# Kernel optimization log

Measured on AMD Instinct MI355X. Metric: run time of the kernel, lower is better.

## Reference

```python
import jax, jax.numpy as jnp
import numpy as np
from jax import lax

EPS = 1e-8

def _conv(x, w, b):
    # x: [B,Cin,H,W], w: [Cout,Cin,kh,kw] (torch OIHW layout), SAME padding, stride 1
    y = lax.conv_general_dilated(x, w, (1, 1), 'SAME',
                                 dimension_numbers=('NCHW', 'OIHW', 'NCHW'))
    return y + b[None, :, None, None]

def setup_inputs() -> dict:
    key = jax.random.key(0)
    ks = jax.random.split(key, 16)
    B, S, H, A, NZ, NO = 256, 4, 32, 5, 150, 17
    d = {
        'map_in': jax.random.uniform(ks[0], (B, 2, H, H), jnp.float32),
        'b0': jax.random.uniform(ks[1], (B, H, H), jnp.float32),
        'act_in': jax.random.randint(ks[2], (B, S), 0, A),
        'obs_in': jax.random.uniform(ks[3], (B, S, 4), jnp.float32),
        'is_start': 1,
        'step_size': S,
        'VI_k': 64,
        # parameters, initialized per the torch init scheme
        'Tb_w': 1.0 / 9.0 + jax.random.normal(ks[4], (A, 1, 3, 3)) / 90.0,
        'Tb_b': jnp.zeros((A,)),
        'Tv_w': 1.0 / 9.0 + jax.random.normal(ks[5], (A, 1, 3, 3)) / 90.0,
        'Tv_b': jnp.zeros((A,)),
        'Z1_w': jax.random.normal(ks[6], (NZ, 1, 3, 3)) / 3.0,
        'Z1_b': jnp.zeros((NZ,)),
        'Z2_w': jax.random.normal(ks[7], (NO, NZ, 1, 1)) / np.sqrt(NZ),
        'Z2_b': jnp.zeros((NO,)),
        'O1_w': jax.random.normal(ks[8], (NO, 4)) * 0.25,
        'O1_b': jnp.zeros((NO,)),
        'O3_w': jax.random.normal(ks[9], (NO, NO)) / NO,
        'O3_b': jnp.zeros((NO,)),
        'R1_w': jax.random.normal(ks[10], (NZ, 2, 3, 3)) / np.sqrt(18.0),
        'R1_b': jnp.zeros((NZ,)),
        'R2_w': jax.random.normal(ks[11], (A, NZ, 1, 1)) / np.sqrt(NZ),
        'R2_b': jnp.zeros((A,)),
        'FL_w': jax.random.normal(ks[12], (A, A)) * 0.25,
        'FL_b': jnp.zeros((A,)),
    }
    return d

def reference(map_in, b0, act_in, obs_in, is_start, step_size, VI_k,
              Tb_w, Tb_b, Tv_w, Tv_b, Z1_w, Z1_b, Z2_w, Z2_b,
              O1_w, O1_b, O3_w, O3_b, R1_w, R1_b, R2_w, R2_b, FL_w, FL_b):
    B, _, H, W = map_in.shape
    A = Tb_w.shape[0]

    # ---- VI: value iteration conv+add+max loop ----
    R = _conv(jax.nn.relu(_conv(map_in, R1_w, R1_b)), R2_w, R2_b)  # [B,A,H,W]
    v0 = jnp.zeros((B, 1, H, W), map_in.dtype)
    Q0 = jnp.zeros_like(R)

    def vi_step(carry, _):
        v, _Q = carry
        Q = _conv(v, Tv_w, Tv_b) + R
        v = jnp.max(Q, axis=1, keepdims=True)
        return (v, Q), None

    (_, Q), _ = lax.scan(vi_step, (v0, Q0), None, length=VI_k)
    Q = jnp.transpose(Q, (0, 2, 3, 1))  # [B,H,W,A]

    # ---- observation model Z ----
    Z = jax.nn.sigmoid(_conv(_conv(map_in[:, :1], Z1_w, Z1_b), Z2_w, Z2_b))
    Z = jnp.transpose(Z, (0, 2, 3, 1))  # [B,H,W,17]
    Z = Z / (jnp.sum(Z, axis=3, keepdims=True) + EPS)

    # ---- recurrent Bayes filter + policy ----
    b = b0 if is_start else b0  # is_start resets belief to b0 (always true here)
    outs = []
    for t in range(step_size):  # small fixed recurrence length
        o = obs_in[:, t]  # [B,4]
        w = jax.nn.softmax(jnp.tanh(o @ O1_w.T + O1_b) @ O3_w.T + O3_b, axis=1)  # [B,17]
        Z_O = jnp.einsum('bhwo,bo->bhw', Z, w)
        bp = jnp.transpose(_conv(b[:, None], Tb_w, Tb_b), (0, 2, 3, 1))  # [B,H,W,A]
        a1h = jax.nn.one_hot(act_in[:, t], A, dtype=bp.dtype)
        b_pa = jnp.einsum('bhwa,ba->bhw', bp, a1h)
        b_next = b_pa * Z_O
        b = b_next / (jnp.sum(b_next, axis=(1, 2), keepdims=True) + EPS)
        Qb = jnp.einsum('bhwa,bhw->ba', Q, b)
        outs.append(Qb @ FL_w.T + FL_b)
    outputs = jnp.concatenate(outs, axis=0)  # [step_size*B, A]
    return outputs, b
```

## Files before the change

kernel.cpp:

```cpp
#include <hip/hip_runtime.h>

#define EPSV 1e-8f
#define PW   34
#define NPIX 1024
#define NA   5
#define NOUT 17
#define NZC  150
#define MAXS 8

__global__ __launch_bounds__(1024, 4) void vin_fused(
    const float* __restrict__ map_in, const float* __restrict__ b0,
    const int*   __restrict__ act_in, const float* __restrict__ obs_in,
    const int*   __restrict__ step_p, const int*   __restrict__ vik_p,
    const float* __restrict__ Tb_w,  const float* __restrict__ Tb_b,
    const float* __restrict__ Tv_w,  const float* __restrict__ Tv_b,
    const float* __restrict__ Z1_w,  const float* __restrict__ Z1_b,
    const float* __restrict__ Z2_w,  const float* __restrict__ Z2_b,
    const float* __restrict__ O1_w,  const float* __restrict__ O1_b,
    const float* __restrict__ O3_w,  const float* __restrict__ O3_b,
    const float* __restrict__ R1_w,  const float* __restrict__ R1_b,
    const float* __restrict__ R2_w,  const float* __restrict__ R2_b,
    const float* __restrict__ FL_w,  const float* __restrict__ FL_b,
    float* __restrict__ out, int B)
{
    __shared__ float map0[PW*PW], map1[PW*PW], v_lds[PW*PW], b_lds[PW*PW];
    __shared__ float zc_w[NOUT*9], zc_b[NOUT];
    __shared__ float h_all[MAXS][NOUT], u_all[MAXS][NOUT], w_all[MAXS][NOUT];
    __shared__ float zo_lds[MAXS * NPIX];
    __shared__ float partials[16][6], sums[6];

    const int tid  = threadIdx.x;
    const int blk  = blockIdx.x;
    const int y    = tid >> 5, x = tid & 31;
    const int pidx = (y + 1) * PW + (x + 1);
    const int lane = tid & 63, wvid = tid >> 6;

    const int S = step_p[0];
    const int K = vik_p[0];

    for (int i = tid; i < PW*PW; i += NPIX) {
        map0[i] = 0.f; map1[i] = 0.f; v_lds[i] = 0.f; b_lds[i] = 0.f;
    }
    __syncthreads();
    map0[pidx]  = map_in[blk*2*NPIX + tid];
    map1[pidx]  = map_in[blk*2*NPIX + NPIX + tid];
    b_lds[pidx] = b0[blk*NPIX + tid];

    if (tid < NOUT*9) {
        const int o = tid / 9, k = tid % 9;
        float s = 0.f;
        for (int c = 0; c < NZC; ++c) s += Z2_w[o*NZC + c] * Z1_w[c*9 + k];
        zc_w[tid] = s;
    } else if (tid < NOUT*9 + NOUT) {
        const int o = tid - NOUT*9;
        float s = Z2_b[o];
        for (int c = 0; c < NZC; ++c) s += Z2_w[o*NZC + c] * Z1_b[c];
        zc_b[o] = s;
    }

    const int mt = tid - 256;
    const int mT = mt / NOUT, mO = mt % NOUT;
    if (mt >= 0 && mt < S*NOUT) {
        const float* ob = obs_in + (blk*S + mT)*4;
        float hh = O1_b[mO];
        #pragma unroll
        for (int k = 0; k < 4; ++k) hh += ob[k] * O1_w[mO*4 + k];
        h_all[mT][mO] = tanhf(hh);
    }
    __syncthreads();
    if (mt >= 0 && mt < S*NOUT) {
        float u = O3_b[mO];
        #pragma unroll
        for (int j = 0; j < NOUT; ++j) u += h_all[mT][j] * O3_w[mO*NOUT + j];
        u_all[mT][mO] = u;
    }
    __syncthreads();
    if (mt >= 0 && mt < S*NOUT) {
        float mx = u_all[mT][0];
        #pragma unroll
        for (int j = 1; j < NOUT; ++j) mx = fmaxf(mx, u_all[mT][j]);
        float sm = 0.f;
        #pragma unroll
        for (int j = 0; j < NOUT; ++j) sm += expf(u_all[mT][j] - mx);
        w_all[mT][mO] = expf(u_all[mT][mO] - mx) / sm;
    }
    __syncthreads();

    float m0[9], m1[9];
    #pragma unroll
    for (int k = 0; k < 9; ++k) {
        const int off = (y + k/3)*PW + x + (k%3);
        m0[k] = map0[off]; m1[k] = map1[off];
    }

    float r[NA];
    #pragma unroll
    for (int a = 0; a < NA; ++a) r[a] = R2_b[a];
    for (int c = 0; c < NZC; ++c) {
        float s = R1_b[c];
        const float* w1 = R1_w + c*18;
        #pragma unroll
        for (int k = 0; k < 9; ++k) s += m0[k] * w1[k];
        #pragma unroll
        for (int k = 0; k < 9; ++k) s += m1[k] * w1[9 + k];
        s = fmaxf(s, 0.f);
        #pragma unroll
        for (int a = 0; a < NA; ++a) r[a] += R2_w[a*NZC + c] * s;
    }

    {
        float z[NOUT];
        float zs = 0.f;
        #pragma unroll
        for (int o = 0; o < NOUT; ++o) {
            float s = zc_b[o];
            #pragma unroll
            for (int k = 0; k < 9; ++k) s += m0[k] * zc_w[o*9 + k];
            const float zz = 1.f / (1.f + expf(-s));
            z[o] = zz; zs += zz;
        }
        const float zn = 1.f / (zs + EPSV);
        for (int t = 0; t < S; ++t) {
            float zo = 0.f;
            #pragma unroll
            for (int o = 0; o < NOUT; ++o) zo += z[o] * w_all[t][o];
            zo_lds[t*NPIX + tid] = zo * zn;
        }
    }

    float q[NA];
    #pragma unroll
    for (int a = 0; a < NA; ++a) q[a] = 0.f;
    for (int it = 0; it < K; ++it) {
        float n[9];
        #pragma unroll
        for (int k = 0; k < 9; ++k) n[k] = v_lds[(y + k/3)*PW + x + (k%3)];
        float vmax = -3.4e38f;
        #pragma unroll
        for (int a = 0; a < NA; ++a) {
            float s = Tv_b[a] + r[a];
            #pragma unroll
            for (int k = 0; k < 9; ++k) s += n[k] * Tv_w[a*9 + k];
            q[a] = s;
            vmax = fmaxf(vmax, s);
        }
        __syncthreads();
        v_lds[pidx] = vmax;
        __syncthreads();
    }

    for (int t = 0; t < S; ++t) {
        const int a_t = act_in[blk*S + t];
        float bp = Tb_b[a_t];
        #pragma unroll
        for (int k = 0; k < 9; ++k)
            bp += b_lds[(y + k/3)*PW + x + (k%3)] * Tb_w[a_t*9 + k];

        const float bn = bp * zo_lds[t*NPIX + tid];

        float v6[6];
        v6[5] = bn;
        #pragma unroll
        for (int a = 0; a < NA; ++a) v6[a] = q[a] * bn;
        #pragma unroll
        for (int k = 0; k < 6; ++k) {
            float vv = v6[k];
            for (int off = 32; off > 0; off >>= 1) vv += __shfl_down(vv, off);
            v6[k] = vv;
        }
        if (lane == 0) {
            #pragma unroll
            for (int k = 0; k < 6; ++k) partials[wvid][k] = v6[k];
        }
        __syncthreads();
        if (tid < 6) {
            float s = 0.f;
            for (int w2 = 0; w2 < 16; ++w2) s += partials[w2][tid];
            sums[tid] = s;
        }
        __syncthreads();

        const float inv = 1.f / (sums[5] + EPSV);
        if (tid < NA) {
            float oj = FL_b[tid];
            #pragma unroll
            for (int a = 0; a < NA; ++a) oj += (sums[a] * inv) * FL_w[tid*NA + a];
            out[(t*B + blk)*NA + tid] = oj;
        }
        b_lds[pidx] = bn * inv;
        __syncthreads();
    }

    out[S*B*NA + blk*NPIX + tid] = b_lds[pidx];
}

extern "C" void kernel_launch(void* const* d_in, const int* in_sizes, int n_in,
                              void* d_out, int out_size, void* d_ws, size_t ws_size,
                              hipStream_t stream)
{
    const float* map_in = (const float*)d_in[0];
    const float* b0     = (const float*)d_in[1];
    const int*   act_in = (const int*)  d_in[2];
    const float* obs_in = (const float*)d_in[3];
    const int*   step_p = (const int*)  d_in[5];
    const int*   vik_p  = (const int*)  d_in[6];
    const float* Tb_w = (const float*)d_in[7];
    const float* Tb_b = (const float*)d_in[8];
    const float* Tv_w = (const float*)d_in[9];
    const float* Tv_b = (const float*)d_in[10];
    const float* Z1_w = (const float*)d_in[11];
    const float* Z1_b = (const float*)d_in[12];
    const float* Z2_w = (const float*)d_in[13];
    const float* Z2_b = (const float*)d_in[14];
    const float* O1_w = (const float*)d_in[15];
    const float* O1_b = (const float*)d_in[16];
    const float* O3_w = (const float*)d_in[17];
    const float* O3_b = (const float*)d_in[18];
    const float* R1_w = (const float*)d_in[19];
    const float* R1_b = (const float*)d_in[20];
    const float* R2_w = (const float*)d_in[21];
    const float* R2_b = (const float*)d_in[22];
    const float* FL_w = (const float*)d_in[23];
    const float* FL_b = (const float*)d_in[24];

    const int B = in_sizes[1] / NPIX;

    hipLaunchKernelGGL(vin_fused, dim3(B), dim3(1024), 0, stream,
        map_in, b0, act_in, obs_in, step_p, vik_p,
        Tb_w, Tb_b, Tv_w, Tv_b, Z1_w, Z1_b, Z2_w, Z2_b,
        O1_w, O1_b, O3_w, O3_b, R1_w, R1_b, R2_w, R2_b,
        FL_w, FL_b, (float*)d_out, B);
}
```

Baseline: 187.9 us.

## Compute two vertically adjacent pixels per thread with double-buffered value map

Halves the block to 512 threads, with each thread computing two vertically stacked pixels. Overlapping stencil loads are shared between the two outputs, and each thread's own center values stay in registers. The value-iteration loop now ping-pongs between two LDS buffers, which cuts it to one barrier per iteration instead of two. Register pressure goes up, and there are fewer threads per block to hide latency.

```diff
diff --git a/kernel.cpp b/kernel.cpp
--- a/kernel.cpp
+++ b/kernel.cpp
@@ -8,7 +8,7 @@
 #define NZC  150
 #define MAXS 8
 
-__global__ __launch_bounds__(1024, 4) void vin_fused(
+__global__ __launch_bounds__(512, 2) void vin_fused(
     const float* __restrict__ map_in, const float* __restrict__ b0,
     const int*   __restrict__ act_in, const float* __restrict__ obs_in,
     const int*   __restrict__ step_p, const int*   __restrict__ vik_p,
@@ -23,28 +23,38 @@
     const float* __restrict__ FL_w,  const float* __restrict__ FL_b,
     float* __restrict__ out, int B)
 {
-    __shared__ float map0[PW*PW], map1[PW*PW], v_lds[PW*PW], b_lds[PW*PW];
+    __shared__ float map0[PW*PW], map1[PW*PW];
+    __shared__ float v_a[PW*PW], v_b[PW*PW], b_lds[PW*PW];
     __shared__ float zc_w[NOUT*9], zc_b[NOUT];
     __shared__ float h_all[MAXS][NOUT], u_all[MAXS][NOUT], w_all[MAXS][NOUT];
     __shared__ float zo_lds[MAXS * NPIX];
-    __shared__ float partials[16][6], sums[6];
+    __shared__ float partials[8][6], sums[6];
 
     const int tid  = threadIdx.x;
     const int blk  = blockIdx.x;
-    const int y    = tid >> 5, x = tid & 31;
-    const int pidx = (y + 1) * PW + (x + 1);
+    const int x    = tid & 31;
+    const int yr   = tid >> 5;
+    const int y0   = yr * 2;
+    const int p0   = y0*32 + x, p1 = p0 + 32;
+    const int bi   = y0*PW + x;
+    const int ci0  = bi + PW + 1;
+    const int ci1  = bi + 2*PW + 1;
     const int lane = tid & 63, wvid = tid >> 6;
 
     const int S = step_p[0];
     const int K = vik_p[0];
 
-    for (int i = tid; i < PW*PW; i += NPIX) {
-        map0[i] = 0.f; map1[i] = 0.f; v_lds[i] = 0.f; b_lds[i] = 0.f;
+    for (int i = tid; i < PW*PW; i += 512) {
+        map0[i] = 0.f; map1[i] = 0.f; v_a[i] = 0.f; v_b[i] = 0.f; b_lds[i] = 0.f;
     }
     __syncthreads();
-    map0[pidx]  = map_in[blk*2*NPIX + tid];
-    map1[pidx]  = map_in[blk*2*NPIX + NPIX + tid];
-    b_lds[pidx] = b0[blk*NPIX + tid];
+    map0[ci0] = map_in[blk*2*NPIX + p0];
+    map0[ci1] = map_in[blk*2*NPIX + p1];
+    map1[ci0] = map_in[blk*2*NPIX + NPIX + p0];
+    map1[ci1] = map_in[blk*2*NPIX + NPIX + p1];
+    float bc0 = b0[blk*NPIX + p0];
+    float bc1 = b0[blk*NPIX + p1];
+    b_lds[ci0] = bc0; b_lds[ci1] = bc1;
 
     if (tid < NOUT*9) {
         const int o = tid / 9, k = tid % 9;
@@ -86,31 +96,36 @@
     }
     __syncthreads();
 
-    float m0[9], m1[9];
+    float m0[12], m1[12];
     #pragma unroll
-    for (int k = 0; k < 9; ++k) {
-        const int off = (y + k/3)*PW + x + (k%3);
-        m0[k] = map0[off]; m1[k] = map1[off];
-    }
-
-    float r[NA];
+    for (int kr = 0; kr < 4; ++kr)
+        #pragma unroll
+        for (int kc = 0; kc < 3; ++kc) {
+            const int off = bi + kr*PW + kc;
+            m0[kr*3+kc] = map0[off]; m1[kr*3+kc] = map1[off];
+        }
+
+    float r0a[NA], r1a[NA];
     #pragma unroll
-    for (int a = 0; a < NA; ++a) r[a] = R2_b[a];
+    for (int a = 0; a < NA; ++a) { r0a[a] = R2_b[a]; r1a[a] = R2_b[a]; }
     for (int c = 0; c < NZC; ++c) {
-        float s = R1_b[c];
         const float* w1 = R1_w + c*18;
-        #pragma unroll
-        for (int k = 0; k < 9; ++k) s += m0[k] * w1[k];
-        #pragma unroll
-        for (int k = 0; k < 9; ++k) s += m1[k] * w1[9 + k];
-        s = fmaxf(s, 0.f);
-        #pragma unroll
-        for (int a = 0; a < NA; ++a) r[a] += R2_w[a*NZC + c] * s;
+        float s0 = R1_b[c], s1 = R1_b[c];
+        #pragma unroll
+        for (int k = 0; k < 9; ++k) { s0 += m0[k]   * w1[k];   s1 += m0[3+k] * w1[k]; }
+        #pragma unroll
+        for (int k = 0; k < 9; ++k) { s0 += m1[k]   * w1[9+k]; s1 += m1[3+k] * w1[9+k]; }
+        s0 = fmaxf(s0, 0.f); s1 = fmaxf(s1, 0.f);
+        #pragma unroll
+        for (int a = 0; a < NA; ++a) {
+            r0a[a] += R2_w[a*NZC + c] * s0;
+            r1a[a] += R2_w[a*NZC + c] * s1;
+        }
     }
 
     {
-        float z[NOUT];
-        float zs = 0.f;
+        float z[NOUT]; float zs;
+        zs = 0.f;
         #pragma unroll
         for (int o = 0; o < NOUT; ++o) {
             float s = zc_b[o];
@@ -119,49 +134,101 @@
             const float zz = 1.f / (1.f + expf(-s));
             z[o] = zz; zs += zz;
         }
-        const float zn = 1.f / (zs + EPSV);
-        for (int t = 0; t < S; ++t) {
-            float zo = 0.f;
+        {
+            const float zn = 1.f / (zs + EPSV);
+            for (int t = 0; t < S; ++t) {
+                float zo = 0.f;
+                #pragma unroll
+                for (int o = 0; o < NOUT; ++o) zo += z[o] * w_all[t][o];
+                zo_lds[t*NPIX + p0] = zo * zn;
+            }
+        }
+        zs = 0.f;
+        #pragma unroll
+        for (int o = 0; o < NOUT; ++o) {
+            float s = zc_b[o];
             #pragma unroll
-            for (int o = 0; o < NOUT; ++o) zo += z[o] * w_all[t][o];
-            zo_lds[t*NPIX + tid] = zo * zn;
-        }
-    }
-
-    float q[NA];
+            for (int k = 0; k < 9; ++k) s += m0[3+k] * zc_w[o*9 + k];
+            const float zz = 1.f / (1.f + expf(-s));
+            z[o] = zz; zs += zz;
+        }
+        {
+            const float zn = 1.f / (zs + EPSV);
+            for (int t = 0; t < S; ++t) {
+                float zo = 0.f;
+                #pragma unroll
+                for (int o = 0; o < NOUT; ++o) zo += z[o] * w_all[t][o];
+                zo_lds[t*NPIX + p1] = zo * zn;
+            }
+        }
+    }
+
+    float q0[NA], q1[NA];
     #pragma unroll
-    for (int a = 0; a < NA; ++a) q[a] = 0.f;
-    for (int it = 0; it < K; ++it) {
-        float n[9];
-        #pragma unroll
-        for (int k = 0; k < 9; ++k) n[k] = v_lds[(y + k/3)*PW + x + (k%3)];
-        float vmax = -3.4e38f;
-        #pragma unroll
-        for (int a = 0; a < NA; ++a) {
-            float s = Tv_b[a] + r[a];
-            #pragma unroll
-            for (int k = 0; k < 9; ++k) s += n[k] * Tv_w[a*9 + k];
-            q[a] = s;
-            vmax = fmaxf(vmax, s);
-        }
-        __syncthreads();
-        v_lds[pidx] = vmax;
-        __syncthreads();
-    }
+    for (int a = 0; a < NA; ++a) {
+        q0[a] = 0.f; q1[a] = 0.f;
+        r0a[a] += Tv_b[a]; r1a[a] += Tv_b[a];
+    }
+    float vc0 = 0.f, vc1 = 0.f;
+
+#define VISTEP(SRC, DST)                                                        \
+    {                                                                           \
+        const float A0 = SRC[bi],        A1 = SRC[bi+1],        A2 = SRC[bi+2]; \
+        const float B0 = SRC[bi+PW],     B2 = SRC[bi+PW+2];                     \
+        const float C0 = SRC[bi+2*PW],   C2 = SRC[bi+2*PW+2];                   \
+        const float D0 = SRC[bi+3*PW],   D1 = SRC[bi+3*PW+1],   D2 = SRC[bi+3*PW+2]; \
+        float vm0 = -3.4e38f, vm1 = -3.4e38f;                                   \
+        _Pragma("unroll")                                                       \
+        for (int a = 0; a < NA; ++a) {                                          \
+            const float* w = Tv_w + a*9;                                        \
+            float s0 = r0a[a];                                                  \
+            s0 += A0*w[0]; s0 += A1*w[1]; s0 += A2*w[2];                        \
+            s0 += B0*w[3]; s0 += vc0*w[4]; s0 += B2*w[5];                       \
+            s0 += C0*w[6]; s0 += vc1*w[7]; s0 += C2*w[8];                       \
+            float s1 = r1a[a];                                                  \
+            s1 += B0*w[0]; s1 += vc0*w[1]; s1 += B2*w[2];                       \
+            s1 += C0*w[3]; s1 += vc1*w[4]; s1 += C2*w[5];                       \
+            s1 += D0*w[6]; s1 += D1*w[7]; s1 += D2*w[8];                        \
+            q0[a] = s0; q1[a] = s1;                                             \
+            vm0 = fmaxf(vm0, s0); vm1 = fmaxf(vm1, s1);                         \
+        }                                                                       \
+        vc0 = vm0; vc1 = vm1;                                                   \
+        DST[ci0] = vm0; DST[ci1] = vm1;                                         \
+        __syncthreads();                                                        \
+    }
+
+    {
+        int it = 0;
+        for (; it + 1 < K; it += 2) { VISTEP(v_a, v_b); VISTEP(v_b, v_a); }
+        if (it < K) { VISTEP(v_a, v_b); }
+    }
+#undef VISTEP
 
     for (int t = 0; t < S; ++t) {
         const int a_t = act_in[blk*S + t];
-        float bp = Tb_b[a_t];
-        #pragma unroll
-        for (int k = 0; k < 9; ++k)
-            bp += b_lds[(y + k/3)*PW + x + (k%3)] * Tb_w[a_t*9 + k];
-
-        const float bn = bp * zo_lds[t*NPIX + tid];
+        const float* tw = Tb_w + a_t*9;
+        const float tb = Tb_b[a_t];
+        float bp0 = tb, bp1 = tb;
+        {
+            const float A0 = b_lds[bi],      A1 = b_lds[bi+1],      A2 = b_lds[bi+2];
+            const float B0 = b_lds[bi+PW],   B2 = b_lds[bi+PW+2];
+            const float C0 = b_lds[bi+2*PW], C2 = b_lds[bi+2*PW+2];
+            const float D0 = b_lds[bi+3*PW], D1 = b_lds[bi+3*PW+1], D2 = b_lds[bi+3*PW+2];
+            bp0 += A0*tw[0]; bp0 += A1*tw[1]; bp0 += A2*tw[2];
+            bp0 += B0*tw[3]; bp0 += bc0*tw[4]; bp0 += B2*tw[5];
+            bp0 += C0*tw[6]; bp0 += bc1*tw[7]; bp0 += C2*tw[8];
+            bp1 += B0*tw[0]; bp1 += bc0*tw[1]; bp1 += B2*tw[2];
+            bp1 += C0*tw[3]; bp1 += bc1*tw[4]; bp1 += C2*tw[5];
+            bp1 += D0*tw[6]; bp1 += D1*tw[7]; bp1 += D2*tw[8];
+        }
+
+        const float bn0 = bp0 * zo_lds[t*NPIX + p0];
+        const float bn1 = bp1 * zo_lds[t*NPIX + p1];
 
         float v6[6];
-        v6[5] = bn;
-        #pragma unroll
-        for (int a = 0; a < NA; ++a) v6[a] = q[a] * bn;
+        v6[5] = bn0 + bn1;
+        #pragma unroll
+        for (int a = 0; a < NA; ++a) v6[a] = q0[a]*bn0 + q1[a]*bn1;
         #pragma unroll
         for (int k = 0; k < 6; ++k) {
             float vv = v6[k];
@@ -175,7 +242,7 @@
         __syncthreads();
         if (tid < 6) {
             float s = 0.f;
-            for (int w2 = 0; w2 < 16; ++w2) s += partials[w2][tid];
+            for (int w2 = 0; w2 < 8; ++w2) s += partials[w2][tid];
             sums[tid] = s;
         }
         __syncthreads();
@@ -187,11 +254,13 @@
             for (int a = 0; a < NA; ++a) oj += (sums[a] * inv) * FL_w[tid*NA + a];
             out[(t*B + blk)*NA + tid] = oj;
         }
-        b_lds[pidx] = bn * inv;
+        bc0 = bn0 * inv; bc1 = bn1 * inv;
+        b_lds[ci0] = bc0; b_lds[ci1] = bc1;
         __syncthreads();
     }
 
-    out[S*B*NA + blk*NPIX + tid] = b_lds[pidx];
+    out[S*B*NA + blk*NPIX + p0] = bc0;
+    out[S*B*NA + blk*NPIX + p1] = bc1;
 }
 
 extern "C" void kernel_launch(void* const* d_in, const int* in_sizes, int n_in,
@@ -225,7 +294,7 @@
 
     const int B = in_sizes[1] / NPIX;
 
-    hipLaunchKernelGGL(vin_fused, dim3(B), dim3(1024), 0, stream,
+    hipLaunchKernelGGL(vin_fused, dim3(B), dim3(512), 0, stream,
         map_in, b0, act_in, obs_in, step_p, vik_p,
         Tb_w, Tb_b, Tv_w, Tv_b, Z1_w, Z1_b, Z2_w, Z2_b,
         O1_w, O1_b, O3_w, O3_b, R1_w, R1_b, R2_w, R2_b,
```

Result: slower. 213.2 us (+13.4%).
